# Performance work log

Measured on AMD Instinct MI355X. Metric: run time of the kernel, lower is better.

## Reference

```python
import jax, jax.numpy as jnp
import numpy as np

B, S, H, D_MODEL, D_HEAD = 2, 2048, 12, 768, 64
INIT_RANGE = 0.02
IGNORE = -100000.0


def setup_inputs() -> dict:
    key = jax.random.key(0)
    ks = jax.random.split(key, 11)
    return {
        "normalized_resid_pre_q": jax.random.normal(ks[0], (B, S, H, D_MODEL), jnp.float32),
        "normalized_resid_pre_k": jax.random.normal(ks[1], (B, S, H, D_MODEL), jnp.float32),
        "normalized_resid_pre_v": jax.random.normal(ks[2], (B, S, H, D_MODEL), jnp.float32),
        "W_Q": jax.random.normal(ks[3], (H, D_MODEL, D_HEAD), jnp.float32) * INIT_RANGE,
        "b_Q": jnp.zeros((H, D_HEAD), jnp.float32),
        "W_K": jax.random.normal(ks[4], (H, D_MODEL, D_HEAD), jnp.float32) * INIT_RANGE,
        "b_K": jnp.zeros((H, D_HEAD), jnp.float32),
        "W_V": jax.random.normal(ks[5], (H, D_MODEL, D_HEAD), jnp.float32) * INIT_RANGE,
        "b_V": jnp.zeros((H, D_HEAD), jnp.float32),
        "W_O": jax.random.normal(ks[6], (H, D_HEAD, D_MODEL), jnp.float32) * INIT_RANGE,
        "b_O": jnp.zeros((D_MODEL,), jnp.float32),
    }


def reference(normalized_resid_pre_q, normalized_resid_pre_k, normalized_resid_pre_v,
              W_Q, b_Q, W_K, b_K, W_V, b_V, W_O, b_O):
    n_heads = W_Q.shape[0]
    d_head = W_Q.shape[-1]
    # per-head projections: input already carries a head axis
    q = jnp.einsum("bqhm,hmd->bqhd", normalized_resid_pre_q, W_Q) + b_Q
    k = jnp.einsum("bkhm,hmd->bkhd", normalized_resid_pre_k, W_K) + b_K
    v = jnp.einsum("bkhm,hmd->bkhd", normalized_resid_pre_v, W_V) + b_V
    scores = jnp.einsum("bqhd,bkhd->bhqk", q, k) / jnp.sqrt(jnp.float32(d_head))
    S_q, S_k = scores.shape[-2], scores.shape[-1]
    causal = jnp.triu(jnp.ones((S_q, S_k), bool), k=1)
    scores = jnp.where(causal, jnp.float32(IGNORE), scores)
    pattern = jax.nn.softmax(scores, axis=-1)
    z = jnp.einsum("bhqk,bkhd->bqhd", pattern, v)
    # output keeps the per-head axis; bias split evenly across heads
    attn_out = jnp.einsum("bqhd,hdm->bqhm", z, W_O) + b_O / n_heads
    return attn_out
```

## Files before the change

### kernel.cpp

```cpp
#include <hip/hip_runtime.h>
#include <hip/hip_bf16.h>
#include <stdint.h>

#define H 12
#define S 2048
#define BATCH 2
#define DM 768
#define DH 64

typedef __attribute__((ext_vector_type(4))) float f32x4;
typedef __attribute__((ext_vector_type(4))) short s16x4;
typedef __attribute__((ext_vector_type(8))) short s16x8;

static __device__ __forceinline__ short f2bf(float f) {
  uint32_t u = __builtin_bit_cast(uint32_t, f);
  uint32_t r = (u + 0x7FFFu + ((u >> 16) & 1u)) >> 16;
  return (short)r;
}

static __device__ __forceinline__ s16x8 cvt8(f32x4 a, f32x4 b) {
  s16x8 r;
  r[0] = f2bf(a[0]); r[1] = f2bf(a[1]); r[2] = f2bf(a[2]); r[3] = f2bf(a[3]);
  r[4] = f2bf(b[0]); r[5] = f2bf(b[1]); r[6] = f2bf(b[2]); r[7] = f2bf(b[3]);
  return r;
}

static __device__ __forceinline__ f32x4 zero4() {
  f32x4 v; v[0] = 0.f; v[1] = 0.f; v[2] = 0.f; v[3] = 0.f; return v;
}

#define GLD_LDS16(g, l)                                                              \
  __builtin_amdgcn_global_load_lds((__attribute__((address_space(1))) const void*)(g), \
                                   (__attribute__((address_space(3))) void*)(l), 16, 0, 0)

#define WAITV(N) asm volatile("s_waitcnt vmcnt(" #N ")" ::: "memory")
#define WAITL0() asm volatile("s_waitcnt lgkmcnt(0)" ::: "memory")
#define BAR() __builtin_amdgcn_s_barrier()
#define FENCE() asm volatile("" ::: "memory")
#define PRIO(N) __builtin_amdgcn_s_setprio(N)

__global__ __launch_bounds__(256) void k_prep(const float* __restrict__ wq,
                                              const float* __restrict__ wk,
                                              const float* __restrict__ wv,
                                              const float* __restrict__ wo,
                                              short* __restrict__ wt,
                                              short* __restrict__ wot) {
  int tid = blockIdx.x * 256 + threadIdx.x;
  int nthr = gridDim.x * 256;
  const int NQKV = 3 * H * DM * DH;
  for (int i = tid; i < NQKV; i += nthr) {
    int n = i & 63;
    int k = (i >> 6) % DM;
    int rest = (i >> 6) / DM;
    int h = rest % H;
    int t = rest / H;
    const float* src = (t == 0 ? wq : t == 1 ? wk : wv);
    float v = src[((size_t)h * DM + k) * DH + n];
    wt[(((size_t)t * H + h) * DH + n) * DM + k] = f2bf(v);
  }
  const int NO = H * DH * DM;
  for (int i = tid; i < NO; i += nthr) {
    int m = i % DM;
    int d = (i / DM) % DH;
    int h = i / (DM * DH);
    wot[((size_t)h * DM + m) * DH + d] = f2bf(wo[((size_t)h * DH + d) * DM + m]);
  }
}

__global__ __launch_bounds__(256) void k_proj(
    const float* __restrict__ xq, const float* __restrict__ xk, const float* __restrict__ xv,
    const float* __restrict__ bq, const float* __restrict__ bk, const float* __restrict__ bv,
    const short* __restrict__ wt,
    short* __restrict__ q_ws, short* __restrict__ k_ws, short* __restrict__ vt_ws) {
  const int u = blockIdx.x;
  const int xcd = u & 7;
  const int slot = u >> 3;
  const int r = (slot / 12) * 8 + xcd;
  const int h = slot % 12;
  const int t = r / 64;
  const int rb = r % 64;
  const int b = rb >> 5;
  const int q0 = (rb & 31) * 64;

  const float* x = (t == 0 ? xq : t == 1 ? xk : xv);
  const float* xbase = x + ((size_t)(b * S + q0) * H + h) * DM;
  const short* wbase = wt + ((size_t)t * H + h) * (size_t)DH * DM;

  __shared__ float A_sm[2][64 * 64];
  __shared__ short W_sm[2][64 * 64];

  const int tid = threadIdx.x;
  const int w = tid >> 6;
  const int l = tid & 63;
  const int g = l >> 4;
  const int m16 = l & 15;
  const int wswz = ((l & 7) ^ (l >> 3)) * 8;

  const int arow_st = (l >> 4);
  const int apb = (l & 15) * 16;

  f32x4 acc[4];
#pragma unroll
  for (int nt = 0; nt < 4; ++nt) acc[nt] = zero4();

#define PROJ_STAGE(sel, kc)                                                          \
  do {                                                                               \
    _Pragma("unroll") for (int i = 0; i < 4; ++i) {                                  \
      int row = (w * 4 + i) * 4 + arow_st;                                           \
      int colf = (apb ^ ((row & 7) << 4)) >> 2;                                      \
      GLD_LDS16(xbase + (size_t)row * (H * DM) + (kc) * 64 + colf,                   \
                (char*)A_sm + (sel) * 16384 + (w * 4 + i) * 1024);                   \
    }                                                                                \
    _Pragma("unroll") for (int i = 0; i < 2; ++i) {                                  \
      int ch = w * 2 + i;                                                            \
      int n = ch * 8 + (l >> 3);                                                     \
      GLD_LDS16(wbase + (size_t)n * DM + (kc) * 64 + wswz,                           \
                (char*)W_sm + (sel) * 8192 + ch * 1024);                             \
    }                                                                                \
  } while (0)

#define PROJ_COMPUTE(sel)                                                            \
  do {                                                                               \
    const char* Ab = (const char*)A_sm + (sel) * 16384;                              \
    const char* Wb = (const char*)W_sm + (sel) * 8192;                               \
    int arow = 16 * w + m16;                                                         \
    int asw = (arow & 7) << 4;                                                       \
    _Pragma("unroll") for (int c = 0; c < 2; ++c) {                                  \
      f32x4 a0 = *(const f32x4*)(Ab + arow * 256 + ((32 * g + 128 * c) ^ asw));      \
      f32x4 a1 = *(const f32x4*)(Ab + arow * 256 + ((32 * g + 128 * c + 16) ^ asw)); \
      s16x8 afr = cvt8(a0, a1);                                                      \
      int krow = 8 * g + 32 * c;                                                     \
      PRIO(1);                                                                       \
      _Pragma("unroll") for (int nt = 0; nt < 4; ++nt) {                             \
        int n = m16 + 16 * nt;                                                       \
        s16x8 bfr = *(const s16x8*)(Wb + ((n * 128 + krow * 2) ^ ((n & 7) << 4)));   \
        acc[nt] = __builtin_amdgcn_mfma_f32_16x16x32_bf16(afr, bfr, acc[nt], 0, 0, 0); \
      }                                                                              \
      PRIO(0);                                                                       \
    }                                                                                \
  } while (0)

  PROJ_STAGE(0, 0);
#pragma unroll
  for (int kc = 0; kc < 12; ++kc) {
    const int cur = kc & 1;
    if (kc < 11) {
      PROJ_STAGE(cur ^ 1, kc + 1);
      WAITV(6);
    } else {
      WAITV(0);
    }
    BAR(); FENCE();
    PROJ_COMPUTE(cur);
    WAITL0(); BAR(); FENCE();
  }

  const float* bias = (t == 0 ? bq : t == 1 ? bk : bv) + h * DH;
  if (t < 2) {
    short* dst = (t == 0 ? q_ws : k_ws) + (size_t)(b * H + h) * S * DH;
#pragma unroll
    for (int nt = 0; nt < 4; ++nt) {
      int n = 16 * nt + m16;
      float bb = bias[n];
#pragma unroll
      for (int r2 = 0; r2 < 4; ++r2) {
        int q = q0 + 16 * w + 4 * g + r2;
        dst[(size_t)q * DH + n] = f2bf(acc[nt][r2] + bb);
      }
    }
  } else {
    short* dst = vt_ws + (size_t)(b * H + h) * DH * S;
#pragma unroll
    for (int nt = 0; nt < 4; ++nt) {
      int n = 16 * nt + m16;
      float bb = bias[n];
#pragma unroll
      for (int r2 = 0; r2 < 4; ++r2) {
        int q = q0 + 16 * w + 4 * g + r2;
        dst[(size_t)n * S + q] = f2bf(acc[nt][r2] + bb);
      }
    }
  }
}

__global__ __launch_bounds__(256) void k_attn_o(const short* __restrict__ q_ws,
                                                const short* __restrict__ k_ws,
                                                const short* __restrict__ vt_ws,
                                                const short* __restrict__ wot,
                                                const float* __restrict__ bo,
                                                float* __restrict__ out) {
  const int u = blockIdx.x;
  const int xcd = u & 7;
  const int slot = u >> 3;
  const int r = (slot / 12) * 8 + xcd;
  const int h = slot % 12;
  const int b = r >> 5;
  const int qtile = 31 - (r & 31);
  const int q0 = qtile * 64;

  const size_t sl = (size_t)(b * H + h) * S * DH;
  const short* qs = q_ws + sl;
  const short* ks = k_ws + sl;
  const short* vs = vt_ws + sl;

  __shared__ short K_sm[2][64 * 64];
  __shared__ short V_sm[2][64 * 64];
  __shared__ short P_sm[4][16 * 72];

  const int tid = threadIdx.x;
  const int w = tid >> 6;
  const int l = tid & 63;
  const int g = l >> 4;
  const int m16 = l & 15;
  const int swz_src = ((l & 7) ^ (l >> 3)) * 8;

#define ATTN_STAGE(sel, kv0)                                                         \
  do {                                                                               \
    _Pragma("unroll") for (int i = 0; i < 2; ++i) {                                  \
      int ch = w * 2 + i;                                                            \
      int row = ch * 8 + (l >> 3);                                                   \
      GLD_LDS16(ks + (size_t)((kv0) + row) * DH + swz_src,                           \
                (char*)K_sm + (sel) * 8192 + ch * 1024);                             \
      GLD_LDS16(vs + (size_t)row * S + (kv0) + swz_src,                              \
                (char*)V_sm + (sel) * 8192 + ch * 1024);                             \
    }                                                                                \
  } while (0)

  s16x8 qf[2];
  {
    int q = q0 + 16 * w + m16;
    qf[0] = *(const s16x8*)(qs + (size_t)q * DH + 8 * g);
    qf[1] = *(const s16x8*)(qs + (size_t)q * DH + 8 * g + 32);
  }

  f32x4 o_acc[4];
  float m_run[4], l_run[4], alpha[4];
#pragma unroll
  for (int nt = 0; nt < 4; ++nt) o_acc[nt] = zero4();
#pragma unroll
  for (int rr = 0; rr < 4; ++rr) { m_run[rr] = -3.0e38f; l_run[rr] = 0.f; }

  const int ktiles = qtile + 1;
  ATTN_STAGE(0, 0);
  for (int kt = 0; kt < ktiles; ++kt) {
    const int kv0 = kt * 64;
    const int cur = kt & 1;
    if (kt + 1 < ktiles) {
      ATTN_STAGE(cur ^ 1, kv0 + 64);
      WAITV(4);
    } else {
      WAITV(0);
    }
    BAR(); FENCE();

    f32x4 sacc[4];
#pragma unroll
    for (int nt = 0; nt < 4; ++nt) sacc[nt] = zero4();
    PRIO(1);
#pragma unroll
    for (int c = 0; c < 2; ++c) {
      int kr2 = (8 * g + 32 * c) * 2;
#pragma unroll
      for (int nt = 0; nt < 4; ++nt) {
        int row = m16 + 16 * nt;
        s16x8 kf = *(const s16x8*)((const char*)K_sm + cur * 8192 +
                                   ((row * 128 + kr2) ^ ((row & 7) << 4)));
        sacc[nt] = __builtin_amdgcn_mfma_f32_16x16x32_bf16(qf[c], kf, sacc[nt], 0, 0, 0);
      }
    }
    PRIO(0);
    float sv[4][4];
#pragma unroll
    for (int nt = 0; nt < 4; ++nt) {
      int kv = kv0 + 16 * nt + m16;
#pragma unroll
      for (int rr = 0; rr < 4; ++rr) {
        int q = q0 + 16 * w + 4 * g + rr;
        float s = sacc[nt][rr] * 0.125f;
        sv[nt][rr] = (kv > q) ? -1.0e30f : s;
      }
    }
#pragma unroll
    for (int rr = 0; rr < 4; ++rr) {
      float tm = fmaxf(fmaxf(sv[0][rr], sv[1][rr]), fmaxf(sv[2][rr], sv[3][rr]));
      tm = fmaxf(tm, __shfl_xor(tm, 1));
      tm = fmaxf(tm, __shfl_xor(tm, 2));
      tm = fmaxf(tm, __shfl_xor(tm, 4));
      tm = fmaxf(tm, __shfl_xor(tm, 8));
      float mn = fmaxf(m_run[rr], tm);
      alpha[rr] = __expf(m_run[rr] - mn);
      m_run[rr] = mn;
      float rs = 0.f;
#pragma unroll
      for (int nt = 0; nt < 4; ++nt) {
        float p = __expf(sv[nt][rr] - mn);
        sv[nt][rr] = p;
        rs += p;
      }
      rs += __shfl_xor(rs, 1);
      rs += __shfl_xor(rs, 2);
      rs += __shfl_xor(rs, 4);
      rs += __shfl_xor(rs, 8);
      l_run[rr] = l_run[rr] * alpha[rr] + rs;
    }
#pragma unroll
    for (int nt = 0; nt < 4; ++nt)
#pragma unroll
      for (int rr = 0; rr < 4; ++rr)
        P_sm[w][(4 * g + rr) * 72 + 16 * nt + m16] = f2bf(sv[nt][rr]);
#pragma unroll
    for (int nt = 0; nt < 4; ++nt)
#pragma unroll
      for (int rr = 0; rr < 4; ++rr) o_acc[nt][rr] *= alpha[rr];
#pragma unroll
    for (int c = 0; c < 2; ++c) {
      s16x8 pf = *(const s16x8*)(&P_sm[w][m16 * 72 + 8 * g + 32 * c]);
      int kv2 = (8 * g + 32 * c) * 2;
      PRIO(1);
#pragma unroll
      for (int nt = 0; nt < 4; ++nt) {
        int d = m16 + 16 * nt;
        s16x8 vf = *(const s16x8*)((const char*)V_sm + cur * 8192 +
                                   ((d * 128 + kv2) ^ ((d & 7) << 4)));
        o_acc[nt] = __builtin_amdgcn_mfma_f32_16x16x32_bf16(pf, vf, o_acc[nt], 0, 0, 0);
      }
      PRIO(0);
    }
    WAITL0(); BAR(); FENCE();
  }

  short* Z_sm = (short*)K_sm;
  char* WO_sm = (char*)V_sm;
  float* bo_lds = (float*)P_sm;
  const short* wos = wot + (size_t)h * DM * DH;

#define STAGE_WO(sel, nc)                                                            \
  do {                                                                               \
    _Pragma("unroll") for (int i = 0; i < 2; ++i) {                                  \
      int ch = w * 2 + i;                                                            \
      int row = ch * 8 + (l >> 3);                                                   \
      GLD_LDS16(wos + (size_t)((nc) * 64 + row) * DH + swz_src,                      \
                WO_sm + (sel) * 8192 + ch * 1024);                                   \
    }                                                                                \
  } while (0)

  STAGE_WO(0, 0);
  for (int i = tid; i < DM; i += 256) bo_lds[i] = bo[i] * (1.0f / 12.0f);
#pragma unroll
  for (int nt = 0; nt < 4; ++nt) {
#pragma unroll
    for (int rr = 0; rr < 4; ++rr) {
      int row = 16 * w + 4 * g + rr;
      int d = 16 * nt + m16;
      int byte = (row * 128 + d * 2) ^ ((row & 7) << 4);
      *(short*)((char*)Z_sm + byte) = f2bf(o_acc[nt][rr] / l_run[rr]);
    }
  }
  WAITL0(); BAR(); FENCE();

  s16x8 af[2];
#pragma unroll
  for (int c = 0; c < 2; ++c) {
    int row = 16 * w + m16;
    int kr2 = (8 * g + 32 * c) * 2;
    af[c] = *(const s16x8*)((const char*)Z_sm + ((row * 128 + kr2) ^ ((row & 7) << 4)));
  }

#pragma unroll
  for (int nc = 0; nc < 12; ++nc) {
    const int cur = nc & 1;
    if (nc < 11) {
      STAGE_WO(cur ^ 1, nc + 1);
      if (nc == 0) { WAITV(2); }
      else        { WAITV(18); }
    } else {
      WAITV(0);
    }
    BAR(); FENCE();
    f32x4 acc[4];
#pragma unroll
    for (int nt = 0; nt < 4; ++nt) acc[nt] = zero4();
    PRIO(1);
#pragma unroll
    for (int c = 0; c < 2; ++c) {
      int kr2 = (8 * g + 32 * c) * 2;
#pragma unroll
      for (int nt = 0; nt < 4; ++nt) {
        int row = m16 + 16 * nt;
        s16x8 bf = *(const s16x8*)(WO_sm + cur * 8192 +
                                   ((row * 128 + kr2) ^ ((row & 7) << 4)));
        acc[nt] = __builtin_amdgcn_mfma_f32_16x16x32_bf16(af[c], bf, acc[nt], 0, 0, 0);
      }
    }
    PRIO(0);
#pragma unroll
    for (int nt = 0; nt < 4; ++nt) {
      int m = nc * 64 + 16 * nt + m16;
      float bias = bo_lds[m];
#pragma unroll
      for (int rr = 0; rr < 4; ++rr) {
        int q = q0 + 16 * w + 4 * g + rr;
        out[((size_t)(b * S + q) * H + h) * DM + m] = acc[nt][rr] + bias;
      }
    }
    WAITL0(); BAR(); FENCE();
  }
#undef STAGE_WO
#undef ATTN_STAGE
}

extern "C" void kernel_launch(void* const* d_in, const int* in_sizes, int n_in,
                              void* d_out, int out_size, void* d_ws, size_t ws_size,
                              hipStream_t stream) {
  const float* xq = (const float*)d_in[0];
  const float* xk = (const float*)d_in[1];
  const float* xv = (const float*)d_in[2];
  const float* wq = (const float*)d_in[3];
  const float* bq = (const float*)d_in[4];
  const float* wk = (const float*)d_in[5];
  const float* bk = (const float*)d_in[6];
  const float* wv = (const float*)d_in[7];
  const float* bv = (const float*)d_in[8];
  const float* wo = (const float*)d_in[9];
  const float* bo = (const float*)d_in[10];
  float* out = (float*)d_out;

  short* wt = (short*)d_ws;
  short* wot = wt + (size_t)3 * H * DH * DM;
  short* q_ws = wot + (size_t)H * DM * DH;
  short* k_ws = q_ws + (size_t)BATCH * H * S * DH;
  short* vt_ws = k_ws + (size_t)BATCH * H * S * DH;

  k_prep<<<dim3(1024), dim3(256), 0, stream>>>(wq, wk, wv, wo, wt, wot);
  k_proj<<<dim3(2304), dim3(256), 0, stream>>>(xq, xk, xv, bq, bk, bv, wt, q_ws, k_ws, vt_ws);
  k_attn_o<<<dim3(768), dim3(256), 0, stream>>>(q_ws, k_ws, vt_ws, wot, bo, out);
}
```

Before: 219.5 us.

## Halve projection row tile and stage activations in larger 256-column chunks

The projection kernel now processes 32 rows per block instead of 64, doubling the grid to 4608 blocks. Each wave computes a 16x32 output sub-tile instead of 16x64. Activations are staged in 256-column chunks that are double-buffered separately from the 64-column weight chunks, with reworked wait counts. The aim is more parallelism and fewer, larger activation loads for this memory-bound fp32 input read. The cost is that weights are re-read twice as often, LDS use per block rises, and MFMA work per barrier falls.

Result: slower. 237.4 us (+8.1%).

```diff
diff --git a/kernel.cpp b/kernel.cpp
--- a/kernel.cpp
+++ b/kernel.cpp
@@ -77,16 +77,16 @@
   const int slot = u >> 3;
   const int r = (slot / 12) * 8 + xcd;
   const int h = slot % 12;
-  const int t = r / 64;
-  const int rb = r % 64;
-  const int b = rb >> 5;
-  const int q0 = (rb & 31) * 64;
+  const int t = r / 128;
+  const int rb = r % 128;
+  const int b = rb >> 6;
+  const int q0 = (rb & 63) * 32;
 
   const float* x = (t == 0 ? xq : t == 1 ? xk : xv);
   const float* xbase = x + ((size_t)(b * S + q0) * H + h) * DM;
   const short* wbase = wt + ((size_t)t * H + h) * (size_t)DH * DM;
 
-  __shared__ float A_sm[2][64 * 64];
+  __shared__ float A_sm[2][32 * 256];
   __shared__ short W_sm[2][64 * 64];
 
   const int tid = threadIdx.x;
@@ -96,91 +96,102 @@
   const int m16 = l & 15;
   const int wswz = ((l & 7) ^ (l >> 3)) * 8;
 
-  const int arow_st = (l >> 4);
-  const int apb = (l & 15) * 16;
-
-  f32x4 acc[4];
-#pragma unroll
-  for (int nt = 0; nt < 4; ++nt) acc[nt] = zero4();
-
-#define PROJ_STAGE(sel, kc)                                                          \
+  const int mt = w & 1;
+  const int nt2 = w >> 1;
+  const int arow = 16 * mt + m16;
+  const int asw = (arow & 7) << 4;
+
+  f32x4 acc[2];
+  acc[0] = zero4(); acc[1] = zero4();
+
+#define STAGE_A(sel, sc)                                                             \
   do {                                                                               \
-    _Pragma("unroll") for (int i = 0; i < 4; ++i) {                                  \
-      int row = (w * 4 + i) * 4 + arow_st;                                           \
-      int colf = (apb ^ ((row & 7) << 4)) >> 2;                                      \
-      GLD_LDS16(xbase + (size_t)row * (H * DM) + (kc) * 64 + colf,                   \
-                (char*)A_sm + (sel) * 16384 + (w * 4 + i) * 1024);                   \
+    _Pragma("unroll") for (int j = 0; j < 8; ++j) {                                  \
+      int rloc = w * 8 + j;                                                          \
+      int colf = ((l * 16) ^ ((rloc & 7) << 4)) >> 2;                                \
+      GLD_LDS16(xbase + (size_t)rloc * (H * DM) + (sc) * 256 + colf,                 \
+                (char*)A_sm + (sel) * 32768 + rloc * 1024);                          \
     }                                                                                \
+  } while (0)
+
+#define STAGE_W(sel, G)                                                              \
+  do {                                                                               \
     _Pragma("unroll") for (int i = 0; i < 2; ++i) {                                  \
       int ch = w * 2 + i;                                                            \
       int n = ch * 8 + (l >> 3);                                                     \
-      GLD_LDS16(wbase + (size_t)n * DM + (kc) * 64 + wswz,                           \
+      GLD_LDS16(wbase + (size_t)n * DM + (G) * 64 + wswz,                            \
                 (char*)W_sm + (sel) * 8192 + ch * 1024);                             \
     }                                                                                \
   } while (0)
 
-#define PROJ_COMPUTE(sel)                                                            \
-  do {                                                                               \
-    const char* Ab = (const char*)A_sm + (sel) * 16384;                              \
-    const char* Wb = (const char*)W_sm + (sel) * 8192;                               \
-    int arow = 16 * w + m16;                                                         \
-    int asw = (arow & 7) << 4;                                                       \
-    _Pragma("unroll") for (int c = 0; c < 2; ++c) {                                  \
-      f32x4 a0 = *(const f32x4*)(Ab + arow * 256 + ((32 * g + 128 * c) ^ asw));      \
-      f32x4 a1 = *(const f32x4*)(Ab + arow * 256 + ((32 * g + 128 * c + 16) ^ asw)); \
-      s16x8 afr = cvt8(a0, a1);                                                      \
-      int krow = 8 * g + 32 * c;                                                     \
-      PRIO(1);                                                                       \
-      _Pragma("unroll") for (int nt = 0; nt < 4; ++nt) {                             \
-        int n = m16 + 16 * nt;                                                       \
-        s16x8 bfr = *(const s16x8*)(Wb + ((n * 128 + krow * 2) ^ ((n & 7) << 4)));   \
-        acc[nt] = __builtin_amdgcn_mfma_f32_16x16x32_bf16(afr, bfr, acc[nt], 0, 0, 0); \
-      }                                                                              \
-      PRIO(0);                                                                       \
-    }                                                                                \
-  } while (0)
-
-  PROJ_STAGE(0, 0);
-#pragma unroll
-  for (int kc = 0; kc < 12; ++kc) {
-    const int cur = kc & 1;
-    if (kc < 11) {
-      PROJ_STAGE(cur ^ 1, kc + 1);
-      WAITV(6);
-    } else {
-      WAITV(0);
-    }
-    BAR(); FENCE();
-    PROJ_COMPUTE(cur);
-    WAITL0(); BAR(); FENCE();
+  STAGE_W(0, 0);
+  STAGE_A(0, 0);
+
+#pragma unroll
+  for (int sc = 0; sc < 3; ++sc) {
+#pragma unroll
+    for (int kcl = 0; kcl < 4; ++kcl) {
+      const int G = sc * 4 + kcl;
+      if (G < 11) STAGE_W((G + 1) & 1, G + 1);
+      if (kcl == 2 && sc < 2) STAGE_A((sc + 1) & 1, sc + 1);
+      if (sc < 2) {
+        if (kcl >= 2) { WAITV(10); } else { WAITV(2); }
+      } else {
+        if (kcl == 3) { WAITV(0); } else { WAITV(2); }
+      }
+      BAR(); FENCE();
+      {
+        const char* Ab = (const char*)A_sm + (sc & 1) * 32768 + arow * 1024;
+        const char* Wb = (const char*)W_sm + (G & 1) * 8192;
+        PRIO(1);
+#pragma unroll
+        for (int c = 0; c < 2; ++c) {
+          int qb = kcl * 256 + 32 * g + 128 * c;
+          f32x4 a0 = *(const f32x4*)(Ab + (qb ^ asw));
+          f32x4 a1 = *(const f32x4*)(Ab + ((qb + 16) ^ asw));
+          s16x8 afr = cvt8(a0, a1);
+          int kr2 = (8 * g + 32 * c) * 2;
+#pragma unroll
+          for (int jn = 0; jn < 2; ++jn) {
+            int n = 32 * nt2 + 16 * jn + m16;
+            s16x8 bfr = *(const s16x8*)(Wb + ((n * 128 + kr2) ^ ((n & 7) << 4)));
+            acc[jn] = __builtin_amdgcn_mfma_f32_16x16x32_bf16(afr, bfr, acc[jn], 0, 0, 0);
+          }
+        }
+        PRIO(0);
+      }
+      WAITL0(); BAR(); FENCE();
+    }
   }
 
   const float* bias = (t == 0 ? bq : t == 1 ? bk : bv) + h * DH;
   if (t < 2) {
     short* dst = (t == 0 ? q_ws : k_ws) + (size_t)(b * H + h) * S * DH;
 #pragma unroll
-    for (int nt = 0; nt < 4; ++nt) {
-      int n = 16 * nt + m16;
+    for (int jn = 0; jn < 2; ++jn) {
+      int n = 32 * nt2 + 16 * jn + m16;
       float bb = bias[n];
 #pragma unroll
       for (int r2 = 0; r2 < 4; ++r2) {
-        int q = q0 + 16 * w + 4 * g + r2;
-        dst[(size_t)q * DH + n] = f2bf(acc[nt][r2] + bb);
+        int q = q0 + 16 * mt + 4 * g + r2;
+        dst[(size_t)q * DH + n] = f2bf(acc[jn][r2] + bb);
       }
     }
   } else {
     short* dst = vt_ws + (size_t)(b * H + h) * DH * S;
 #pragma unroll
-    for (int nt = 0; nt < 4; ++nt) {
-      int n = 16 * nt + m16;
+    for (int jn = 0; jn < 2; ++jn) {
+      int n = 32 * nt2 + 16 * jn + m16;
       float bb = bias[n];
 #pragma unroll
       for (int r2 = 0; r2 < 4; ++r2) {
-        int q = q0 + 16 * w + 4 * g + r2;
-        dst[(size_t)n * S + q] = f2bf(acc[nt][r2] + bb);
-      }
-    }
-  }
+        int q = q0 + 16 * mt + 4 * g + r2;
+        dst[(size_t)n * S + q] = f2bf(acc[jn][r2] + bb);
+      }
+    }
+  }
+#undef STAGE_A
+#undef STAGE_W
 }
 
 __global__ __launch_bounds__(256) void k_attn_o(const short* __restrict__ q_ws,
@@ -432,6 +443,6 @@
   short* vt_ws = k_ws + (size_t)BATCH * H * S * DH;
 
   k_prep<<<dim3(1024), dim3(256), 0, stream>>>(wq, wk, wv, wo, wt, wot);
-  k_proj<<<dim3(2304), dim3(256), 0, stream>>>(xq, xk, xv, bq, bk, bv, wt, q_ws, k_ws, vt_ws);
+  k_proj<<<dim3(4608), dim3(256), 0, stream>>>(xq, xk, xv, bq, bk, bv, wt, q_ws, k_ws, vt_ws);
   k_attn_o<<<dim3(768), dim3(256), 0, stream>>>(q_ws, k_ws, vt_ws, wot, bo, out);
 }
```
